# Kernel optimization log

Hardware: AMD Instinct MI355X
Metric: run time of the kernel (lower is better)

## Reference

```python
import jax, jax.numpy as jnp
import numpy as np
from jax.scipy.special import logsumexp

B, T, V, D, HD, L = 64, 512, 100000, 300, 256, 9
H = HD // 2  # per-direction hidden size


def _lstm_dir(x, w_ih, w_hh, b_ih, b_hh, reverse):
    # x: [T, B, in]; PyTorch LSTM gate order: i, f, g, o
    xp = jnp.einsum('tbd,gd->tbg', x, w_ih) + b_ih + b_hh  # [T,B,4H]

    def step(carry, xt):
        h, c = carry
        g = xt + h @ w_hh.T
        i, f, gg, o = jnp.split(g, 4, axis=-1)
        c = jax.nn.sigmoid(f) * c + jax.nn.sigmoid(i) * jnp.tanh(gg)
        h = jax.nn.sigmoid(o) * jnp.tanh(c)
        return (h, c), h

    Bn = x.shape[1]
    init = (jnp.zeros((Bn, H), x.dtype), jnp.zeros((Bn, H), x.dtype))
    _, hs = jax.lax.scan(step, init, xp, reverse=reverse)
    return hs  # [T,B,H]


def _bilstm_layer(x, w_ih, w_hh, b_ih, b_hh):
    hf = _lstm_dir(x, w_ih[0], w_hh[0], b_ih[0], b_hh[0], False)
    hb = _lstm_dir(x, w_ih[1], w_hh[1], b_ih[1], b_hh[1], True)
    return jnp.concatenate([hf, hb], axis=-1)  # [T,B,2H]


def _crf_nll(em, tags, mask, start_t, end_t, trans):
    # em: [B,T,L] emissions; torchcrf log-likelihood with reduction='sum'
    mf = mask.astype(em.dtype)
    em_sel = jnp.take_along_axis(em, tags[:, :, None], axis=2)[..., 0]  # [B,T]
    num = start_t[tags[:, 0]] + em_sel[:, 0]
    tr = trans[tags[:, :-1], tags[:, 1:]]  # [B,T-1]
    num = num + ((tr + em_sel[:, 1:]) * mf[:, 1:]).sum(axis=1)
    seq_ends = mask.sum(axis=1) - 1
    last_tags = jnp.take_along_axis(tags, seq_ends[:, None], axis=1)[:, 0]
    num = num + end_t[last_tags]

    # log-partition via scan over time
    alpha0 = start_t[None, :] + em[:, 0]  # [B,L]

    def step(alpha, inp):
        em_t, m_t = inp  # [B,L], [B]
        nxt = logsumexp(alpha[:, :, None] + trans[None] + em_t[:, None, :], axis=1)
        return jnp.where(m_t[:, None], nxt, alpha), None

    alpha, _ = jax.lax.scan(step, alpha0,
                            (em[:, 1:].transpose(1, 0, 2), mask[:, 1:].T))
    denom = logsumexp(alpha + end_t[None, :], axis=1)
    llh = (num - denom).sum()
    return -llh  # model returns -loss (NLL)


def setup_inputs() -> dict:
    key = jax.random.key(0)
    ks = jax.random.split(key, 18)
    w = lambda k, s: jax.random.normal(k, s, dtype=jnp.float32) * 0.08
    inp = {
        'word_batch': jax.random.randint(ks[0], (B, T), 1, V),  # >=1 so mask is all-true
        'label_batch': jax.random.randint(ks[1], (B, T), 0, L),
        'emb': jax.random.normal(ks[2], (V, D), dtype=jnp.float32) * 0.1,
        'w_ih_l0': w(ks[3], (2, 4 * H, D)),
        'w_hh_l0': w(ks[4], (2, 4 * H, H)),
        'b_ih_l0': w(ks[5], (2, 4 * H)),
        'b_hh_l0': w(ks[6], (2, 4 * H)),
        'w_ih_l1': w(ks[7], (2, 4 * H, HD)),
        'w_hh_l1': w(ks[8], (2, 4 * H, H)),
        'b_ih_l1': w(ks[9], (2, 4 * H)),
        'b_hh_l1': w(ks[10], (2, 4 * H)),
        'w_out': w(ks[11], (L, HD)),
        'b_out': w(ks[12], (L,)),
        'start_t': w(ks[13], (L,)),
        'end_t': w(ks[14], (L,)),
        'trans': w(ks[15], (L, L)),
    }
    return inp


def reference(word_batch, label_batch, emb,
              w_ih_l0, w_hh_l0, b_ih_l0, b_hh_l0,
              w_ih_l1, w_hh_l1, b_ih_l1, b_hh_l1,
              w_out, b_out, start_t, end_t, trans):
    mask = word_batch > 0  # [B,T], all-true by construction
    x = emb[word_batch].transpose(1, 0, 2)  # [T,B,D] (dropout is eval no-op)
    x = _bilstm_layer(x, w_ih_l0, w_hh_l0, b_ih_l0, b_hh_l0)
    x = _bilstm_layer(x, w_ih_l1, w_hh_l1, b_ih_l1, b_hh_l1)
    em = jnp.einsum('tbh,lh->btl', x, w_out) + b_out  # [B,T,L]
    return _crf_nll(em, label_batch, mask, start_t, end_t, trans)
```

## Files before the change

kernel.cpp:

```cpp
#include <hip/hip_runtime.h>

#define TT 512
#define NB 64
#define HH 128
#define G4 512
#define HDIM 256

typedef __bf16 bf16x8 __attribute__((ext_vector_type(8)));
typedef float f32x4 __attribute__((ext_vector_type(4)));
typedef unsigned int u32x4 __attribute__((ext_vector_type(4)));
typedef unsigned int u32x2 __attribute__((ext_vector_type(2)));

union FragU { u32x4 u4; bf16x8 bf; unsigned short us[8]; };
union XPU { u32x2 v; unsigned short us[4]; };

#define SC_SIG  -1.442695041f
#define SC_TANH -2.885390082f

__device__ __forceinline__ unsigned short f2bf(float f){
  unsigned u = __builtin_bit_cast(unsigned, f);
  return (unsigned short)((u + 0x7FFFu + ((u>>16)&1u)) >> 16);
}
__device__ __forceinline__ float bf2f(unsigned short h){
  unsigned u = ((unsigned)h) << 16;
  return __builtin_bit_cast(float, u);
}
__device__ __forceinline__ float rsig(float y){
  return __builtin_amdgcn_rcpf(1.0f + __builtin_amdgcn_exp2f(y));
}


__global__ __launch_bounds__(256) void k_prep(
    const float* __restrict__ bi0, const float* __restrict__ bh0,
    const float* __restrict__ bi1, const float* __restrict__ bh1,
    const float* __restrict__ w_ih0, const float* __restrict__ w_ih1,
    float* __restrict__ bias0, float* __restrict__ bias1,
    unsigned short* __restrict__ Bp0, unsigned short* __restrict__ Bp1)
{
  int id = blockIdx.x*256 + threadIdx.x;
  if (id < 2048){
    int n = id & 511;
    float s = ((n >> 7) == 2) ? SC_TANH : SC_SIG;
    if (id < 1024) bias0[id] = (bi0[id] + bh0[id]) * s;
    else { int k = id - 1024; bias1[k] = (bi1[k] + bh1[k]) * s; }
    return;
  }
  id -= 2048;
  if (id < 320*1024){
    int k = id >> 10, c = id & 1023;
    int dir = c >> 9, n = c & 511;
    float s = ((n >> 7) == 2) ? SC_TANH : SC_SIG;
    float v = (k < 300) ? w_ih0[((size_t)(dir*512 + n))*300 + k] * s : 0.f;
    Bp0[(((size_t)(k>>3))*1024 + c)*8 + (k&7)] = f2bf(v);
    return;
  }
  id -= 320*1024;
  if (id < 256*1024){
    int k = id >> 10, c = id & 1023;
    int dir = c >> 9, n = c & 511;
    float s = ((n >> 7) == 2) ? SC_TANH : SC_SIG;
    float v = w_ih1[((size_t)(dir*512 + n))*256 + k] * s;
    Bp1[(((size_t)(k>>3))*1024 + c)*8 + (k&7)] = f2bf(v);
  }
}

__global__ __launch_bounds__(320) void k_embed(
    const int* __restrict__ word, const float* __restrict__ emb,
    unsigned short* __restrict__ xe)
{
  int row = blockIdx.x;
  int c = threadIdx.x;
  int t = row >> 6, b = row & 63;
  int wd = word[b*TT + t];
  float v = (c < 300) ? emb[(size_t)wd*300 + c] : 0.f;
  xe[(size_t)row*320 + c] = f2bf(v);
}


__global__ __launch_bounds__(256) void k_gemm(
    const unsigned short* __restrict__ A,
    const unsigned short* __restrict__ Bp,
    const float* __restrict__ bias,
    unsigned short* __restrict__ xp,
    const int lda, const int KB)
{
  const int tid = threadIdx.x;
  const int l = tid & 63, w = tid >> 6;
  const int quad = l >> 4, lo = l & 15;
  const int wm = w >> 1, wn = w & 1;
  const int M0 = blockIdx.x * 128;
  const int N0 = blockIdx.y * 128;

  __shared__ __align__(16) unsigned short Asl[4*128*8];
  __shared__ __align__(16) unsigned short Bsl[4*128*8];

  f32x4 acc[4][4] = {};

  for (int kb=0; kb<KB; ++kb){
    const int k0 = kb*32;
    u32x4 va[2], vb[2];
    #pragma unroll
    for (int hh=0; hh<2; ++hh){
      const int cch = tid + hh*256;
      const int q = cch >> 7, mm = cch & 127;
      va[hh] = *(const u32x4*)(A + (size_t)(M0+mm)*lda + k0 + q*8);
      vb[hh] = *(const u32x4*)(Bp + (((size_t)((k0>>3)+q))*1024 + N0 + mm)*8);
    }
    __syncthreads();
    #pragma unroll
    for (int hh=0; hh<2; ++hh){
      const int cch = tid + hh*256;
      *(u32x4*)&Asl[cch*8] = va[hh];
      *(u32x4*)&Bsl[cch*8] = vb[hh];
    }
    __syncthreads();

    FragU af[4], bfg[4];
    #pragma unroll
    for (int mt=0; mt<4; ++mt)
      af[mt].u4 = *(const u32x4*)&Asl[((quad<<7) + wm*64 + mt*16 + lo)*8];
    #pragma unroll
    for (int nt=0; nt<4; ++nt)
      bfg[nt].u4 = *(const u32x4*)&Bsl[((quad<<7) + wn*64 + nt*16 + lo)*8];
    #pragma unroll
    for (int mt=0; mt<4; ++mt)
      #pragma unroll
      for (int nt=0; nt<4; ++nt)
        acc[mt][nt] = __builtin_amdgcn_mfma_f32_16x16x32_bf16(af[mt].bf, bfg[nt].bf, acc[mt][nt], 0, 0, 0);
  }

  #pragma unroll
  for (int mt=0; mt<4; ++mt){
    #pragma unroll
    for (int nt=0; nt<4; ++nt){
      const int col = N0 + wn*64 + nt*16 + lo;
      const int dir = col >> 9, n = col & 511;
      const int g = n >> 7, u = n & 127;
      const float bv = bias[col];
      #pragma unroll
      for (int r=0; r<4; ++r){
        const int row = M0 + wm*64 + mt*16 + quad*4 + r;
        const size_t o = (size_t)row*1024 + dir*512 + u*4 + g;
        xp[o] = f2bf(acc[mt][nt][r] + bv);
      }
    }
  }
}


__global__ __launch_bounds__(256, 1) void k_scan(
    const float* __restrict__ w_hh,
    const unsigned short* __restrict__ xp,
    unsigned short* __restrict__ xout)
{
  const int bid = blockIdx.x;
  const int dir = bid >> 5, bg = bid & 31;
  const int tid = threadIdx.x;
  const int l = tid & 63, w = tid >> 6;
  const int quad = l >> 4, lo = l & 15;
  const int qb = quad >> 1;
  const int qh = quad & 1;
  const int uu = w*32 + qh*16 + lo;
  const int bglob = bg*2 + qb;

  FragU bw[8][4];
  {
    const float* wb = w_hh + (size_t)dir*G4*HH;
    #pragma unroll
    for (int nt=0; nt<8; ++nt){
      const int g = nt >> 1;
      const float s = (g == 2) ? SC_TANH : SC_SIG;
      const int grow = g*HH + w*32 + (nt&1)*16 + lo;
      #pragma unroll
      for (int kq=0; kq<4; ++kq){
        const float* p = wb + (size_t)grow*HH + kq*32 + quad*8;
        #pragma unroll
        for (int j=0; j<8; ++j) bw[nt][kq].us[j] = f2bf(p[j] * s);
      }
    }
  }

  __shared__ __align__(16) unsigned short hbuf[2][2][160];
  for (int i = tid; i < 2*2*160; i += 256) ((unsigned short*)hbuf)[i] = 0;
  __syncthreads();

  float c = 0.f;
  const int t0 = dir ? (TT-1) : 0;
  const int dt = dir ? -1 : 1;
  const unsigned short* xpb = xp + (size_t)bglob*1024 + dir*512 + uu*4;
  unsigned short* xob = xout + (size_t)bglob*HDIM + dir*HH + uu;

  u32x2 cur[4], nxt[4];
  #pragma unroll
  for (int k=0; k<4; ++k)
    cur[k] = *(const u32x2*)(xpb + (size_t)(t0 + dt*k)*65536);

  unsigned short h4[4];
  const f32x4 zero4 = {0.f, 0.f, 0.f, 0.f};

  for (int ob=0; ob<TT/4; ++ob){
    #pragma unroll
    for (int ph=0; ph<4; ++ph){
      const int rb = ph & 1;
      const int wb2 = rb ^ 1;

      FragU af[4];
      #pragma unroll
      for (int kq=0; kq<4; ++kq)
        af[kq].u4 = *(const u32x4*)&hbuf[rb][lo >> 3][kq*32 + quad*8];

      if (ph == 0){
        if (ob){
          #pragma unroll
          for (int k=0; k<4; ++k){
            const int ts = t0 + dt*((ob-1)*4 + k);
            xob[(size_t)ts*NB*HDIM] = h4[k];
          }
        }
        #pragma unroll
        for (int k=0; k<4; ++k){
          int itn = (ob+1)*4 + k; if (itn > TT-1) itn = TT-1;
          nxt[k] = *(const u32x2*)(xpb + (size_t)(t0 + dt*itn)*65536);
        }
      }

      f32x4 acc[8];
      #pragma unroll
      for (int nt=0; nt<8; ++nt)
        acc[nt] = __builtin_amdgcn_mfma_f32_16x16x32_bf16(af[0].bf, bw[nt][0].bf, zero4, 0, 0, 0);
      #pragma unroll
      for (int kq=1; kq<4; ++kq)
        #pragma unroll
        for (int nt=0; nt<8; ++nt)
          acc[nt] = __builtin_amdgcn_mfma_f32_16x16x32_bf16(af[kq].bf, bw[nt][kq].bf, acc[nt], 0, 0, 0);

      XPU xu; xu.v = cur[ph];

      float gv[4];
      #pragma unroll
      for (int g=0; g<4; ++g)
        gv[g] = (qh ? acc[g*2+1][0] : acc[g*2][0]) + bf2f(xu.us[g]);

      float si = rsig(gv[0]), sf = rsig(gv[1]);
      float tg = __builtin_fmaf(2.0f, rsig(gv[2]), -1.0f);
      float so = rsig(gv[3]);
      c = __builtin_fmaf(sf, c, si*tg);
      float h = so * __builtin_fmaf(2.0f, rsig(SC_TANH*c), -1.0f);
      unsigned short hb = f2bf(h);
      h4[ph] = hb;
      hbuf[wb2][qb][uu] = hb;

      asm volatile("s_waitcnt lgkmcnt(0)\n\ts_barrier" ::: "memory");
    }
    #pragma unroll
    for (int k=0; k<4; ++k) cur[k] = nxt[k];
  }

  #pragma unroll
  for (int k=0; k<4; ++k){
    const int ts = t0 + dt*((TT/4 - 1)*4 + k);
    xob[(size_t)ts*NB*HDIM] = h4[k];
  }
}


__global__ __launch_bounds__(256) void k_em(
    const unsigned short* __restrict__ x2,
    const float* __restrict__ w_out,
    const float* __restrict__ b_out,
    float* __restrict__ em)
{
  const int tid = threadIdx.x;
  const int l = tid & 63, w = tid >> 6;
  const int quad = l >> 4, lo = l & 15;
  const int M0 = blockIdx.x*128 + w*32;

  FragU bf[8];
  #pragma unroll
  for (int kq=0; kq<8; ++kq){
    #pragma unroll
    for (int j=0; j<8; ++j){
      float v = (lo < 9) ? w_out[lo*HDIM + kq*32 + quad*8 + j] : 0.f;
      bf[kq].us[j] = f2bf(v);
    }
  }

  f32x4 acc[2] = {};
  #pragma unroll
  for (int kq=0; kq<8; ++kq){
    FragU a0, a1;
    a0.u4 = *(const u32x4*)(x2 + ((size_t)(M0 + lo))*HDIM + kq*32 + quad*8);
    a1.u4 = *(const u32x4*)(x2 + ((size_t)(M0 + 16 + lo))*HDIM + kq*32 + quad*8);
    acc[0] = __builtin_amdgcn_mfma_f32_16x16x32_bf16(a0.bf, bf[kq].bf, acc[0], 0, 0, 0);
    acc[1] = __builtin_amdgcn_mfma_f32_16x16x32_bf16(a1.bf, bf[kq].bf, acc[1], 0, 0, 0);
  }

  if (lo < 9){
    const float bo = b_out[lo];
    #pragma unroll
    for (int mt=0; mt<2; ++mt){
      #pragma unroll
      for (int r=0; r<4; ++r){
        const int row = M0 + mt*16 + quad*4 + r;
        const int t = row >> 6, b = row & 63;
        em[((size_t)b*TT + t)*9 + lo] = acc[mt][r] + bo;
      }
    }
  }
}


__global__ __launch_bounds__(128) void k_crf_r1f(
    const int* __restrict__ word, const float* __restrict__ em,
    const float* __restrict__ start_t, const float* __restrict__ trans,
    float* __restrict__ dst)
{
  const int bid = blockIdx.x;
  const int b = bid >> 6, g = bid & 63;
  const int tid = threadIdx.x;
  const int t0 = g*8;
  __shared__ float R[2][81];
  __shared__ float emsh[8][9];
  __shared__ int wsh[8];
  if (tid < 72){
    int s = tid/9, j = tid - (tid/9)*9;
    emsh[s][j] = em[((size_t)b*TT + t0+s)*9 + j];
  }
  if (tid < 8) wsh[tid] = word[b*TT + t0 + tid];
  __syncthreads();
  int i=0, j=0; float tr[9];
  if (tid < 81){
    i = tid/9; j = tid - i*9;
    #pragma unroll
    for (int k=0;k<9;++k) tr[k] = trans[k*9+j];
    float v;
    if (t0 == 0) v = start_t[j] + emsh[0][j];
    else if (wsh[0] > 0) v = tr[i] + emsh[0][j];
    else v = (i==j) ? 0.f : -1e30f;
    R[0][tid] = v;
  }
  int cur = 0;
  for (int s=1; s<8; ++s){
    __syncthreads();
    if (tid < 81){
      if (wsh[s] > 0){
        float a[9], mx = -3.0e38f;
        #pragma unroll
        for (int k=0;k<9;++k){ a[k] = R[cur][i*9+k] + tr[k]; mx = fmaxf(mx, a[k]); }
        float sm = 0.f;
        #pragma unroll
        for (int k=0;k<9;++k) sm += __expf(a[k]-mx);
        R[cur^1][tid] = mx + __logf(sm) + emsh[s][j];
      } else {
        R[cur^1][tid] = R[cur][tid];
      }
    }
    cur ^= 1;
  }
  __syncthreads();
  if (tid < 81) dst[((size_t)bid)*81 + tid] = R[cur][tid];
}

__global__ __launch_bounds__(128) void k_crf_reduce(
    const float* __restrict__ src, float* __restrict__ dst, const int nm)
{
  const int bid = blockIdx.x;
  const int ng = nm >> 3;
  const int b = bid / ng, g = bid - b*ng;
  const int tid = threadIdx.x;
  __shared__ float R[2][81];
  const float* base = src + ((size_t)b*nm + g*8)*81;
  if (tid < 81) R[0][tid] = base[tid];
  int cur = 0;
  for (int s=1; s<8; ++s){
    __syncthreads();
    if (tid < 81){
      int i = tid/9, j = tid - (tid/9)*9;
      const float* M = base + (size_t)s*81;
      float a[9], mx = -3.0e38f;
      #pragma unroll
      for (int k=0;k<9;++k){ a[k] = R[cur][i*9+k] + M[k*9+j]; mx = fmaxf(mx, a[k]); }
      float sm = 0.f;
      #pragma unroll
      for (int k=0;k<9;++k) sm += __expf(a[k]-mx);
      R[cur^1][tid] = mx + __logf(sm);
    }
    cur ^= 1;
  }
  __syncthreads();
  if (tid < 81) dst[((size_t)b*ng + g)*81 + tid] = R[cur][tid];
}

__global__ __launch_bounds__(256) void k_crf_num(
    const int* __restrict__ word, const int* __restrict__ label,
    const float* __restrict__ em, const float* __restrict__ start_t,
    const float* __restrict__ end_t, const float* __restrict__ trans,
    float* __restrict__ numv)
{
  const int b = blockIdx.x, tid = threadIdx.x;
  __shared__ float sred[256];
  __shared__ int ssend;
  int ms = 0;
  for (int t=tid; t<TT; t+=256) ms += (word[b*TT+t] > 0) ? 1 : 0;
  sred[tid] = (float)ms;
  __syncthreads();
  for (int st=128; st>0; st>>=1){ if (tid<st) sred[tid] += sred[tid+st]; __syncthreads(); }
  if (tid==0) ssend = (int)sred[0] - 1;
  __syncthreads();
  const int send = ssend;
  float part = 0.f;
  for (int t=tid; t<TT; t+=256){
    int tag = label[b*TT+t];
    float es = em[((size_t)b*TT+t)*9 + tag];
    if (t == 0) part += start_t[tag] + es;
    else if (word[b*TT+t] > 0) part += trans[label[b*TT+t-1]*9 + tag] + es;
    if (t == send) part += end_t[tag];
  }
  __syncthreads();
  sred[tid] = part;
  __syncthreads();
  for (int st=128; st>0; st>>=1){ if (tid<st) sred[tid] += sred[tid+st]; __syncthreads(); }
  if (tid==0) numv[b] = sred[0];
}

__global__ __launch_bounds__(64) void k_final(
    const float* __restrict__ numv, const float* __restrict__ G3,
    const float* __restrict__ end_t, float* __restrict__ out)
{
  const int b = threadIdx.x;
  float a[9], mx = -3.0e38f;
  #pragma unroll
  for (int j=0;j<9;++j){ a[j] = G3[b*81 + j] + end_t[j]; mx = fmaxf(mx, a[j]); }
  float sm = 0.f;
  #pragma unroll
  for (int j=0;j<9;++j) sm += __expf(a[j]-mx);
  float denom = mx + __logf(sm);
  float v = numv[b] - denom;
  #pragma unroll
  for (int off=32; off>0; off>>=1) v += __shfl_down(v, off, 64);
  if (b == 0) out[0] = -v;
}


extern "C" void kernel_launch(void* const* d_in, const int* in_sizes, int n_in,
                              void* d_out, int out_size, void* d_ws, size_t ws_size,
                              hipStream_t stream)
{
  (void)in_sizes; (void)n_in; (void)out_size; (void)ws_size;
  const int*   word  = (const int*)d_in[0];
  const int*   label = (const int*)d_in[1];
  const float* emb   = (const float*)d_in[2];
  const float* w_ih0 = (const float*)d_in[3];
  const float* w_hh0 = (const float*)d_in[4];
  const float* b_ih0 = (const float*)d_in[5];
  const float* b_hh0 = (const float*)d_in[6];
  const float* w_ih1 = (const float*)d_in[7];
  const float* w_hh1 = (const float*)d_in[8];
  const float* b_ih1 = (const float*)d_in[9];
  const float* b_hh1 = (const float*)d_in[10];
  const float* w_out = (const float*)d_in[11];
  const float* b_out = (const float*)d_in[12];
  const float* start_t = (const float*)d_in[13];
  const float* end_t   = (const float*)d_in[14];
  const float* trans   = (const float*)d_in[15];

  char* ws = (char*)d_ws;
  unsigned short* xp    = (unsigned short*)(ws + 0);
  unsigned short* xe    = (unsigned short*)(ws + 67108864);
  unsigned short* x1    = (unsigned short*)(ws + 88080384);
  unsigned short* x2    = (unsigned short*)(ws + 104857600);
  unsigned short* Bp0   = (unsigned short*)(ws + 121634816);
  unsigned short* Bp1   = (unsigned short*)(ws + 122290176);
  float*          bias0 = (float*)(ws + 122814464);
  float*          bias1 = (float*)(ws + 122818560);
  float*          em    = (float*)(ws + 122822656);
  float*          G1    = (float*)(ws + 124002304);
  float*          G2    = (float*)(ws + 125329408);
  float*          G3    = (float*)(ws + 125495296);
  float*          numv  = (float*)(ws + 125516032);

  hipLaunchKernelGGL(k_prep, dim3(2312), dim3(256), 0, stream,
                     b_ih0, b_hh0, b_ih1, b_hh1, w_ih0, w_ih1, bias0, bias1, Bp0, Bp1);
  hipLaunchKernelGGL(k_embed, dim3(32768), dim3(320), 0, stream, word, emb, xe);
  hipLaunchKernelGGL(k_gemm, dim3(256, 8), dim3(256), 0, stream, xe, Bp0, bias0, xp, 320, 10);
  hipLaunchKernelGGL(k_scan, dim3(64), dim3(256), 0, stream, w_hh0, xp, x1);
  hipLaunchKernelGGL(k_gemm, dim3(256, 8), dim3(256), 0, stream, x1, Bp1, bias1, xp, 256, 8);
  hipLaunchKernelGGL(k_scan, dim3(64), dim3(256), 0, stream, w_hh1, xp, x2);
  hipLaunchKernelGGL(k_em, dim3(256), dim3(256), 0, stream, x2, w_out, b_out, em);
  hipLaunchKernelGGL(k_crf_r1f, dim3(4096), dim3(128), 0, stream, word, em, start_t, trans, G1);
  hipLaunchKernelGGL(k_crf_reduce, dim3(512), dim3(128), 0, stream, G1, G2, 64);
  hipLaunchKernelGGL(k_crf_reduce, dim3(64), dim3(128), 0, stream, G2, G3, 8);
  hipLaunchKernelGGL(k_crf_num, dim3(64), dim3(256), 0, stream, word, label, em, start_t, end_t, trans, numv);
  hipLaunchKernelGGL(k_final, dim3(1), dim3(64), 0, stream, numv, G3, end_t, (float*)d_out);
}
```

Before: 889.6 us.

## Interleave two independent batch groups per scan block to hide recurrence latency

Each scan block now advances two independent batch pairs (A and B) at once, so the grid shrinks from 64 to 32 blocks. The MFMA chains and gate math of the two pairs interleave, which lets one group's work hide the other's latency on the serial LSTM recurrence, and the per-step barrier is shared by both. The xp prefetch becomes a rolling per-phase load, and the h outputs are now written every step instead of being batched every four steps. The cost is twice the work per step on the critical path, higher register pressure, and half as many CUs in use.

```diff
diff --git a/kernel.cpp b/kernel.cpp
--- a/kernel.cpp
+++ b/kernel.cpp
@@ -154,14 +154,15 @@
     unsigned short* __restrict__ xout)
 {
   const int bid = blockIdx.x;
-  const int dir = bid >> 5, bg = bid & 31;
+  const int dir = bid >> 4, pg = bid & 15;
   const int tid = threadIdx.x;
   const int l = tid & 63, w = tid >> 6;
   const int quad = l >> 4, lo = l & 15;
   const int qb = quad >> 1;
   const int qh = quad & 1;
   const int uu = w*32 + qh*16 + lo;
-  const int bglob = bg*2 + qb;
+  const int bA = pg*4 + qb;
+  const int bB = pg*4 + 2 + qb;
 
   FragU bw[8][4];
   {
@@ -180,86 +181,99 @@
     }
   }
 
-  __shared__ __align__(16) unsigned short hbuf[2][2][160];
-  for (int i = tid; i < 2*2*160; i += 256) ((unsigned short*)hbuf)[i] = 0;
-  __syncthreads();
-
-  float c = 0.f;
+  __shared__ __align__(16) unsigned short hbuf[2][2][2][160];
+  for (int i = tid; i < 2*2*2*160; i += 256) ((unsigned short*)hbuf)[i] = 0;
+  __syncthreads();
+
+  float cA = 0.f, cB = 0.f;
   const int t0 = dir ? (TT-1) : 0;
   const int dt = dir ? -1 : 1;
-  const unsigned short* xpb = xp + (size_t)bglob*1024 + dir*512 + uu*4;
-  unsigned short* xob = xout + (size_t)bglob*HDIM + dir*HH + uu;
-
-  u32x2 cur[4], nxt[4];
-  #pragma unroll
-  for (int k=0; k<4; ++k)
-    cur[k] = *(const u32x2*)(xpb + (size_t)(t0 + dt*k)*65536);
-
-  unsigned short h4[4];
+  const unsigned short* xpA = xp + (size_t)bA*1024 + dir*512 + uu*4;
+  const unsigned short* xpB = xp + (size_t)bB*1024 + dir*512 + uu*4;
+  unsigned short* xoA = xout + (size_t)bA*HDIM + dir*HH + uu;
+  unsigned short* xoB = xout + (size_t)bB*HDIM + dir*HH + uu;
+
+  u32x2 pfA[4], pfB[4];
+  #pragma unroll
+  for (int k=0; k<4; ++k){
+    pfA[k] = *(const u32x2*)(xpA + (size_t)(t0 + dt*k)*65536);
+    pfB[k] = *(const u32x2*)(xpB + (size_t)(t0 + dt*k)*65536);
+  }
+
   const f32x4 zero4 = {0.f, 0.f, 0.f, 0.f};
 
   for (int ob=0; ob<TT/4; ++ob){
     #pragma unroll
     for (int ph=0; ph<4; ++ph){
+      const int it = ob*4 + ph;
+      const int t = t0 + dt*it;
       const int rb = ph & 1;
       const int wb2 = rb ^ 1;
 
-      FragU af[4];
+      FragU afA[4], afB[4];
       #pragma unroll
       for (int kq=0; kq<4; ++kq)
-        af[kq].u4 = *(const u32x4*)&hbuf[rb][lo >> 3][kq*32 + quad*8];
-
-      if (ph == 0){
-        if (ob){
-          #pragma unroll
-          for (int k=0; k<4; ++k){
-            const int ts = t0 + dt*((ob-1)*4 + k);
-            xob[(size_t)ts*NB*HDIM] = h4[k];
-          }
-        }
-        #pragma unroll
-        for (int k=0; k<4; ++k){
-          int itn = (ob+1)*4 + k; if (itn > TT-1) itn = TT-1;
-          nxt[k] = *(const u32x2*)(xpb + (size_t)(t0 + dt*itn)*65536);
-        }
-      }
-
-      f32x4 acc[8];
+        afA[kq].u4 = *(const u32x4*)&hbuf[0][rb][lo >> 3][kq*32 + quad*8];
+      #pragma unroll
+      for (int kq=0; kq<4; ++kq)
+        afB[kq].u4 = *(const u32x4*)&hbuf[1][rb][lo >> 3][kq*32 + quad*8];
+
+      f32x4 accA[8], accB[8];
       #pragma unroll
       for (int nt=0; nt<8; ++nt)
-        acc[nt] = __builtin_amdgcn_mfma_f32_16x16x32_bf16(af[0].bf, bw[nt][0].bf, zero4, 0, 0, 0);
-      #pragma unroll
-      for (int kq=1; kq<4; ++kq)
+        accA[nt] = __builtin_amdgcn_mfma_f32_16x16x32_bf16(afA[0].bf, bw[nt][0].bf, zero4, 0, 0, 0);
+      #pragma unroll
+      for (int nt=0; nt<8; ++nt)
+        accB[nt] = __builtin_amdgcn_mfma_f32_16x16x32_bf16(afB[0].bf, bw[nt][0].bf, zero4, 0, 0, 0);
+      #pragma unroll
+      for (int kq=1; kq<4; ++kq){
         #pragma unroll
         for (int nt=0; nt<8; ++nt)
-          acc[nt] = __builtin_amdgcn_mfma_f32_16x16x32_bf16(af[kq].bf, bw[nt][kq].bf, acc[nt], 0, 0, 0);
-
-      XPU xu; xu.v = cur[ph];
-
-      float gv[4];
-      #pragma unroll
-      for (int g=0; g<4; ++g)
-        gv[g] = (qh ? acc[g*2+1][0] : acc[g*2][0]) + bf2f(xu.us[g]);
-
-      float si = rsig(gv[0]), sf = rsig(gv[1]);
-      float tg = __builtin_fmaf(2.0f, rsig(gv[2]), -1.0f);
-      float so = rsig(gv[3]);
-      c = __builtin_fmaf(sf, c, si*tg);
-      float h = so * __builtin_fmaf(2.0f, rsig(SC_TANH*c), -1.0f);
-      unsigned short hb = f2bf(h);
-      h4[ph] = hb;
-      hbuf[wb2][qb][uu] = hb;
+          accA[nt] = __builtin_amdgcn_mfma_f32_16x16x32_bf16(afA[kq].bf, bw[nt][kq].bf, accA[nt], 0, 0, 0);
+        #pragma unroll
+        for (int nt=0; nt<8; ++nt)
+          accB[nt] = __builtin_amdgcn_mfma_f32_16x16x32_bf16(afB[kq].bf, bw[nt][kq].bf, accB[nt], 0, 0, 0);
+      }
+
+      XPU xuA; xuA.v = pfA[ph];
+      XPU xuB; xuB.v = pfB[ph];
+      {
+        const int itp = (it+4 < TT) ? (it+4) : (TT-1);
+        pfA[ph] = *(const u32x2*)(xpA + (size_t)(t0 + dt*itp)*65536);
+        pfB[ph] = *(const u32x2*)(xpB + (size_t)(t0 + dt*itp)*65536);
+      }
+
+      {
+        float gv[4];
+        #pragma unroll
+        for (int g=0; g<4; ++g)
+          gv[g] = (qh ? accA[g*2+1][0] : accA[g*2][0]) + bf2f(xuA.us[g]);
+        float si = rsig(gv[0]), sf = rsig(gv[1]);
+        float tg = __builtin_fmaf(2.0f, rsig(gv[2]), -1.0f);
+        float so = rsig(gv[3]);
+        cA = __builtin_fmaf(sf, cA, si*tg);
+        float h = so * __builtin_fmaf(2.0f, rsig(SC_TANH*cA), -1.0f);
+        unsigned short hb = f2bf(h);
+        hbuf[0][wb2][qb][uu] = hb;
+        xoA[(size_t)t*NB*HDIM] = hb;
+      }
+      {
+        float gv[4];
+        #pragma unroll
+        for (int g=0; g<4; ++g)
+          gv[g] = (qh ? accB[g*2+1][0] : accB[g*2][0]) + bf2f(xuB.us[g]);
+        float si = rsig(gv[0]), sf = rsig(gv[1]);
+        float tg = __builtin_fmaf(2.0f, rsig(gv[2]), -1.0f);
+        float so = rsig(gv[3]);
+        cB = __builtin_fmaf(sf, cB, si*tg);
+        float h = so * __builtin_fmaf(2.0f, rsig(SC_TANH*cB), -1.0f);
+        unsigned short hb = f2bf(h);
+        hbuf[1][wb2][qb][uu] = hb;
+        xoB[(size_t)t*NB*HDIM] = hb;
+      }
 
       asm volatile("s_waitcnt lgkmcnt(0)\n\ts_barrier" ::: "memory");
     }
-    #pragma unroll
-    for (int k=0; k<4; ++k) cur[k] = nxt[k];
-  }
-
-  #pragma unroll
-  for (int k=0; k<4; ++k){
-    const int ts = t0 + dt*((TT/4 - 1)*4 + k);
-    xob[(size_t)ts*NB*HDIM] = h4[k];
   }
 }
 
@@ -483,9 +497,9 @@
                      b_ih0, b_hh0, b_ih1, b_hh1, w_ih0, w_ih1, bias0, bias1, Bp0, Bp1);
   hipLaunchKernelGGL(k_embed, dim3(32768), dim3(320), 0, stream, word, emb, xe);
   hipLaunchKernelGGL(k_gemm, dim3(256, 8), dim3(256), 0, stream, xe, Bp0, bias0, xp, 320, 10);
-  hipLaunchKernelGGL(k_scan, dim3(64), dim3(256), 0, stream, w_hh0, xp, x1);
+  hipLaunchKernelGGL(k_scan, dim3(32), dim3(256), 0, stream, w_hh0, xp, x1);
   hipLaunchKernelGGL(k_gemm, dim3(256, 8), dim3(256), 0, stream, x1, Bp1, bias1, xp, 256, 8);
-  hipLaunchKernelGGL(k_scan, dim3(64), dim3(256), 0, stream, w_hh1, xp, x2);
+  hipLaunchKernelGGL(k_scan, dim3(32), dim3(256), 0, stream, w_hh1, xp, x2);
   hipLaunchKernelGGL(k_em, dim3(256), dim3(256), 0, stream, x2, w_out, b_out, em);
   hipLaunchKernelGGL(k_crf_r1f, dim3(4096), dim3(128), 0, stream, word, em, start_t, trans, G1);
   hipLaunchKernelGGL(k_crf_reduce, dim3(512), dim3(128), 0, stream, G1, G2, 64);
```

New measurement: 1.188 ms. +33.5%, slower.
